# Kernel tuning notes

Measured on AMD Instinct MI355X. Metric: run time of the kernel, lower is better.

The kernel has to match this reference:

```python
import jax, jax.numpy as jnp
import numpy as np

N = 100000   # nodes
E = 1600000  # edges
D_IN = 4
D_H = 128
EPS = 1e-5

def setup_inputs() -> dict:
    key = jax.random.key(0)
    ks = jax.random.split(key, 4)
    x = jax.random.normal(ks[0], (N, D_IN), dtype=jnp.float32)
    edge_index = jax.random.randint(ks[1], (2, E), 0, N, dtype=jnp.int32)
    W0 = jax.random.normal(ks[2], (D_IN, D_H), dtype=jnp.float32) * 0.5
    b0 = jnp.zeros((D_H,), jnp.float32)
    W12 = jax.random.normal(ks[3], (2, D_H, D_H), dtype=jnp.float32) * (1.0 / np.sqrt(D_H))
    b12 = jnp.zeros((2, D_H), jnp.float32)
    gamma = jnp.ones((3, D_H), jnp.float32)   # GraphNorm weight
    beta = jnp.zeros((3, D_H), jnp.float32)   # GraphNorm bias
    alpha = jnp.ones((3, D_H), jnp.float32)   # GraphNorm mean_scale
    return dict(x=x, edge_index=edge_index, W0=W0, b0=b0, W12=W12, b12=b12,
                gamma=gamma, beta=beta, alpha=alpha)

def gcn_conv(x, src, dst, dinv, W, b):
    # PyG GCNConv: linear first, then D^-1/2 (A+I) D^-1/2 aggregation, bias after.
    h = x @ W                                  # [N, d_out]
    coef = dinv[src] * dinv[dst]               # [E]
    msg = h[src] * coef[:, None]               # [E, d_out] gather
    agg = jax.ops.segment_sum(msg, dst, num_segments=N)  # scatter-add
    agg = agg + h * (dinv * dinv)[:, None]     # self-loop contribution
    return agg + b

def graph_norm(x, g, be, a):
    # single-graph GraphNorm: gamma*(x - alpha*mu)/sqrt(E[(x-alpha*mu)^2]+eps)+beta
    mu = x.mean(axis=0)
    xc = x - a * mu
    var = (xc * xc).mean(axis=0)
    return g * xc * jax.lax.rsqrt(var + EPS) + be

def reference(x, edge_index, W0, b0, W12, b12, gamma, beta, alpha):
    src, dst = edge_index[0], edge_index[1]
    # degree with self loops (edge weight 1)
    deg = jax.ops.segment_sum(jnp.ones((E,), x.dtype), dst, num_segments=N) + 1.0
    dinv = jax.lax.rsqrt(deg)
    h = jax.nn.relu(graph_norm(gcn_conv(x, src, dst, dinv, W0, b0),
                               gamma[0], beta[0], alpha[0]))
    for i in range(2):  # fixed small layer loop
        h = jax.nn.relu(graph_norm(gcn_conv(h, src, dst, dinv, W12[i], b12[i]),
                                   gamma[i + 1], beta[i + 1], alpha[i + 1]))
    return h
```

## Files before the change

### kernel.cpp

```cpp
#include <hip/hip_runtime.h>


#define EPS_GN 1e-5f

typedef __attribute__((ext_vector_type(8))) short bf16x8;
typedef __attribute__((ext_vector_type(4))) float f32x4;

__device__ __forceinline__ float blo(unsigned u) { return __uint_as_float(u << 16); }
__device__ __forceinline__ float bhi(unsigned u) { return __uint_as_float(u & 0xffff0000u); }
__device__ __forceinline__ unsigned bf16rne(float f) {
  unsigned u = __float_as_uint(f);
  u += 0x7fff + ((u >> 16) & 1);
  return u >> 16;
}
__device__ __forceinline__ unsigned packbf(float x, float y) {
  return bf16rne(x) | (bf16rne(y) << 16);
}


__global__ __launch_bounds__(256) void k_count_p(const int* __restrict__ dst,
                                                 int* __restrict__ cnt, int E, int N) {
  int p = blockIdx.x & 7;
  int lo = (int)((long long)N * p >> 3), hi = (int)((long long)N * (p + 1) >> 3);
  int stride = (gridDim.x >> 3) * 256;
  for (int e = (blockIdx.x >> 3) * 256 + threadIdx.x; e < E; e += stride) {
    int d = dst[e];
    if (d >= lo && d < hi) atomicAdd(&cnt[d], 1);
  }
}

__global__ __launch_bounds__(256) void k_scan1(const int* __restrict__ cnt,
                                               int* __restrict__ rs,
                                               int* __restrict__ bsum, int N) {
  __shared__ int s[256];
  int t = threadIdx.x;
  int base = blockIdx.x * 1024 + t * 4;
  int c0 = (base + 0 < N) ? cnt[base + 0] : 0;
  int c1 = (base + 1 < N) ? cnt[base + 1] : 0;
  int c2 = (base + 2 < N) ? cnt[base + 2] : 0;
  int c3 = (base + 3 < N) ? cnt[base + 3] : 0;
  int tsum = c0 + c1 + c2 + c3;
  s[t] = tsum;
  __syncthreads();
  for (int off = 1; off < 256; off <<= 1) {
    int v = (t >= off) ? s[t - off] : 0;
    __syncthreads();
    s[t] += v;
    __syncthreads();
  }
  int excl = s[t] - tsum;
  if (t == 255) bsum[blockIdx.x] = s[255];
  int e0 = excl, e1 = e0 + c0, e2 = e1 + c1, e3 = e2 + c2;
  if (base + 0 < N) rs[base + 0] = e0;
  if (base + 1 < N) rs[base + 1] = e1;
  if (base + 2 < N) rs[base + 2] = e2;
  if (base + 3 < N) rs[base + 3] = e3;
}

__global__ __launch_bounds__(256) void k_scan2(const int* __restrict__ bsum,
                                               int* __restrict__ boff, int nblk) {
  __shared__ int s[256];
  int t = threadIdx.x;
  int v0 = (t < nblk) ? bsum[t] : 0;
  s[t] = v0;
  __syncthreads();
  for (int off = 1; off < 256; off <<= 1) {
    int v = (t >= off) ? s[t - off] : 0;
    __syncthreads();
    s[t] += v;
    __syncthreads();
  }
  if (t < nblk) boff[t] = s[t] - v0;
}

__global__ __launch_bounds__(256) void k_finalize(const int* __restrict__ cnt,
                                                  const int* __restrict__ boff,
                                                  int* __restrict__ rs,
                                                  int* __restrict__ cursor,
                                                  float* __restrict__ dinv, int N, int E) {
  int i = blockIdx.x * 256 + threadIdx.x;
  if (i == 0) rs[N] = E;
  if (i < N) {
    int v = rs[i] + boff[i >> 10];
    rs[i] = v;
    cursor[i] = v;
    dinv[i] = rsqrtf((float)cnt[i] + 1.0f);
  }
}

__global__ __launch_bounds__(256) void k_fill_p(const int* __restrict__ src,
                                                const int* __restrict__ dst,
                                                int* __restrict__ cursor,
                                                int* __restrict__ csr, int E, int N) {
  int p = blockIdx.x & 7;
  int lo = (int)((long long)N * p >> 3), hi = (int)((long long)N * (p + 1) >> 3);
  int stride = (gridDim.x >> 3) * 256;
  for (int e = (blockIdx.x >> 3) * 256 + threadIdx.x; e < E; e += stride) {
    int d = dst[e];
    if (d >= lo && d < hi) {
      int pos = atomicAdd(&cursor[d], 1);
      csr[pos] = src[e];
    }
  }
}


__global__ __launch_bounds__(256) void k_wt(const float* __restrict__ W12,
                                            unsigned short* __restrict__ WbT) {
  int o = blockIdx.x * 256 + threadIdx.x;
  int layer = o >> 14, r = o & 16383;
  int n = r >> 7, k = r & 127;
  WbT[o] = (unsigned short)bf16rne(W12[layer * 16384 + k * 128 + n]);
}


__global__ __launch_bounds__(256) void k_gemm0(const float* __restrict__ X,
                                               const float* __restrict__ W,
                                               const float* __restrict__ dinv,
                                               unsigned* __restrict__ H, int N) {
  __shared__ float Ws[4 * 128];
  int t = threadIdx.x;
  if (t < 128) {
    Ws[t] = W[t];
    Ws[128 + t] = W[128 + t];
    Ws[256 + t] = W[256 + t];
    Ws[384 + t] = W[384 + t];
  }
  __syncthreads();
  int r = t >> 6, l = t & 63;
  int row = blockIdx.x * 4 + r;
  if (row >= N) return;
  float4 xv = ((const float4*)X)[row];
  float di = dinv[row];
  int c0 = 2 * l, c1 = 2 * l + 1;
  float v0 = xv.x * Ws[c0] + xv.y * Ws[128 + c0] + xv.z * Ws[256 + c0] + xv.w * Ws[384 + c0];
  float v1 = xv.x * Ws[c1] + xv.y * Ws[128 + c1] + xv.z * Ws[256 + c1] + xv.w * Ws[384 + c1];
  H[(size_t)row * 64 + l] = packbf(di * v0, di * v1);
}

__global__ __launch_bounds__(256, 4) void k_gemm_mfma(const unsigned* __restrict__ AGGb,
                                                      const unsigned short* __restrict__ WbT,
                                                      const float* __restrict__ stats,
                                                      const float* __restrict__ bias,
                                                      const float* __restrict__ gamma,
                                                      const float* __restrict__ beta,
                                                      const float* __restrict__ alpha,
                                                      const float* __restrict__ dinv,
                                                      unsigned* __restrict__ H, int N,
                                                      float invN) {
  __shared__ float As[128], Bs[128];
  int t = threadIdx.x;
  if (t < 128) {
    float s1 = stats[t] * invN, s2 = stats[128 + t] * invN;
    float b = bias[t], a = alpha[t], g = gamma[t], be = beta[t];
    float mu = s1 + b;
    float E2 = s2 + 2.f * b * s1 + b * b;
    float var = E2 - (2.f * a - a * a) * mu * mu;
    float A = g * rsqrtf(var + EPS_GN);
    As[t] = A;
    Bs[t] = be - A * a * mu + A * b;
  }
  __syncthreads();
  int wv = t >> 6, l = t & 63;
  int r0 = blockIdx.x * 64 + wv * 16;
  if (r0 >= N) return;
  int m = l & 15, kb = l >> 4;

  f32x4 acc[8];
#pragma unroll
  for (int nt = 0; nt < 8; ++nt) acc[nt] = (f32x4){0.f, 0.f, 0.f, 0.f};

  const uint4* Arow = (const uint4*)(AGGb + (size_t)(r0 + m) * 64);

#pragma unroll
  for (int ks = 0; ks < 4; ++ks) {
    int k0 = ks * 32 + kb * 8;
    uint4 a_raw = Arow[ks * 4 + kb];
    float4 A0 = *reinterpret_cast<const float4*>(&As[k0]);
    float4 A1 = *reinterpret_cast<const float4*>(&As[k0 + 4]);
    float4 B0 = *reinterpret_cast<const float4*>(&Bs[k0]);
    float4 B1 = *reinterpret_cast<const float4*>(&Bs[k0 + 4]);
    bf16x8 bf[8];
#pragma unroll
    for (int nt = 0; nt < 8; ++nt)
      bf[nt] = *reinterpret_cast<const bf16x8*>(WbT + (size_t)(nt * 16 + m) * 128 + k0);
    float xr[8] = {blo(a_raw.x), bhi(a_raw.x), blo(a_raw.y), bhi(a_raw.y),
                   blo(a_raw.z), bhi(a_raw.z), blo(a_raw.w), bhi(a_raw.w)};
    float Aa[8] = {A0.x, A0.y, A0.z, A0.w, A1.x, A1.y, A1.z, A1.w};
    float Bb[8] = {B0.x, B0.y, B0.z, B0.w, B1.x, B1.y, B1.z, B1.w};
    bf16x8 af;
#pragma unroll
    for (int j = 0; j < 8; ++j) {
      float v = fmaf(Aa[j], xr[j], Bb[j]);
      v = v > 0.f ? v : 0.f;
      af[j] = (short)bf16rne(v);
    }
#pragma unroll
    for (int nt = 0; nt < 8; ++nt)
      acc[nt] = __builtin_amdgcn_mfma_f32_16x16x32_bf16(af, bf[nt], acc[nt], 0, 0, 0);
  }

  float dn[4];
#pragma unroll
  for (int r = 0; r < 4; ++r) dn[r] = dinv[r0 + kb * 4 + r];
  bool even = (l & 1) == 0;
#pragma unroll
  for (int nt = 0; nt < 8; ++nt) {
#pragma unroll
    for (int r = 0; r < 4; ++r) {
      float v = acc[nt][r] * dn[r];
      float pv = __shfl_xor(v, 1);
      if (even) {
        unsigned word = packbf(v, pv);
        H[(size_t)(r0 + kb * 4 + r) * 64 + nt * 8 + (m >> 1)] = word;
      }
    }
  }
}

__global__ __launch_bounds__(256) void k_gather(const uint4* __restrict__ H4,
                                                const int* __restrict__ rs,
                                                const int* __restrict__ csr,
                                                const float* __restrict__ dinv,
                                                unsigned* __restrict__ AGGb,
                                                float* __restrict__ stats, int N) {
  int wave = threadIdx.x >> 6, lane = threadIdx.x & 63;
  int g = lane >> 4, sl = lane & 15;
  float s1a = 0.f, s1b = 0.f, s2a = 0.f, s2b = 0.f;
  for (int n = blockIdx.x * 4 + wave; n < N; n += gridDim.x * 4) {
    int j0 = rs[n], j1 = rs[n + 1];
    int len = j1 - j0;
    int nb = (len + 4) >> 2;
    float acc[8];
#pragma unroll
    for (int i = 0; i < 8; ++i) acc[i] = 0.f;

    auto vsrc = [&](int b) -> int {
      int idx = b * 4 + g - 1;
      int jj = j0 + idx;
      jj = min(jj, j1 - 1);
      jj = max(jj, j0);
      int c = csr[jj];
      return (idx < 0) ? n : ((idx < len) ? c : N);
    };

    uint4 hA = H4[(size_t)vsrc(0) * 16 + sl];
    uint4 hB, hC, hD, hE;
    if (nb > 1) hB = H4[(size_t)vsrc(1) * 16 + sl];
    if (nb > 2) hC = H4[(size_t)vsrc(2) * 16 + sl];
    if (nb > 3) hD = H4[(size_t)vsrc(3) * 16 + sl];
    for (int b = 0; b < nb; ++b) {
      if (b + 4 < nb) hE = H4[(size_t)vsrc(b + 4) * 16 + sl];
      unsigned uu[4] = {hA.x, hA.y, hA.z, hA.w};
#pragma unroll
      for (int i = 0; i < 4; ++i) {
        acc[2 * i] += blo(uu[i]);
        acc[2 * i + 1] += bhi(uu[i]);
      }
      hA = hB;
      hB = hC;
      hC = hD;
      hD = hE;
    }
#pragma unroll
    for (int i = 0; i < 8; ++i) {
      acc[i] += __shfl_xor(acc[i], 16);
      acc[i] += __shfl_xor(acc[i], 32);
    }
    float dnv = dinv[n];
    float v0 = acc[2 * g] * dnv;
    float v1 = acc[2 * g + 1] * dnv;
    AGGb[(size_t)n * 64 + sl * 4 + g] = packbf(v0, v1);
    s1a += v0;
    s2a = fmaf(v0, v0, s2a);
    s1b += v1;
    s2b = fmaf(v1, v1, s2b);
  }
  __shared__ float sh[4][256];
  int col = sl * 8 + g * 2;
  sh[wave][col] = s1a;
  sh[wave][col + 1] = s1b;
  sh[wave][128 + col] = s2a;
  sh[wave][128 + col + 1] = s2b;
  __syncthreads();
  int t = threadIdx.x;
  float v = sh[0][t] + sh[1][t] + sh[2][t] + sh[3][t];
  atomicAdd(&stats[t], v);
}

__global__ __launch_bounds__(256) void k_norm(const unsigned* __restrict__ AGGb,
                                              const float* __restrict__ stats,
                                              const float* __restrict__ bias,
                                              const float* __restrict__ gamma,
                                              const float* __restrict__ beta,
                                              const float* __restrict__ alpha,
                                              float* __restrict__ OUT, int N, float invN) {
  int i = blockIdx.x * 256 + threadIdx.x;
  if (i >= N * 32) return;
  int c4 = i & 31;
  uint2 u = ((const uint2*)AGGb)[i];
  float vv[4] = {blo(u.x), bhi(u.x), blo(u.y), bhi(u.y)};
  float ov[4];
#pragma unroll
  for (int j = 0; j < 4; ++j) {
    int c = c4 * 4 + j;
    float s1 = stats[c] * invN, s2 = stats[128 + c] * invN;
    float b = bias[c], a = alpha[c], g = gamma[c], be = beta[c];
    float mu = s1 + b;
    float E2 = s2 + 2.f * b * s1 + b * b;
    float var = E2 - (2.f * a - a * a) * mu * mu;
    float A = g * rsqrtf(var + EPS_GN);
    float B = be - A * a * mu + A * b;
    float o = fmaf(A, vv[j], B);
    ov[j] = o > 0.f ? o : 0.f;
  }
  ((float4*)OUT)[i] = make_float4(ov[0], ov[1], ov[2], ov[3]);
}


extern "C" void kernel_launch(void* const* d_in, const int* in_sizes, int n_in,
                              void* d_out, int out_size, void* d_ws, size_t ws_size,
                              hipStream_t stream) {
  const float* x = (const float*)d_in[0];
  const int* ei = (const int*)d_in[1];
  const float* W0 = (const float*)d_in[2];
  const float* b0 = (const float*)d_in[3];
  const float* W12 = (const float*)d_in[4];
  const float* b12 = (const float*)d_in[5];
  const float* gamma = (const float*)d_in[6];
  const float* beta = (const float*)d_in[7];
  const float* alpha = (const float*)d_in[8];
  float* out = (float*)d_out;

  int N = in_sizes[0] / 4;
  int E = in_sizes[1] / 2;
  const int* srcArr = ei;
  const int* dstArr = ei + E;

  char* w = (char*)d_ws;
  auto alloc = [&](size_t bytes) {
    char* p = w;
    w += (bytes + 255) & ~(size_t)255;
    return p;
  };
  int* cnt = (int*)alloc((size_t)N * 4);
  float* stats = (float*)alloc(3 * 256 * 4);
  int* rs = (int*)alloc(((size_t)N + 1) * 4);
  int* cursor = (int*)alloc((size_t)N * 4);
  int* bsum = (int*)alloc(512);
  int* boff = (int*)alloc(512);
  unsigned short* WbT = (unsigned short*)alloc(2 * 16384 * 2);
  int* csr = (int*)alloc(((size_t)E + 8) * 4);
  float* dinv = (float*)alloc((size_t)N * 4);
  unsigned* Hb = (unsigned*)alloc(((size_t)N + 1) * 64 * 4);
  unsigned* AGGb = (unsigned*)alloc((size_t)N * 64 * 4);

  size_t zlen = (size_t)((char*)stats - (char*)cnt) + 3 * 256 * 4;
  hipMemsetAsync(cnt, 0, zlen, stream);
  hipMemsetAsync(Hb + (size_t)N * 64, 0, 256, stream);

  int nblk = (N + 1023) / 1024;
  k_wt<<<128, 256, 0, stream>>>(W12, WbT);
  k_count_p<<<2048, 256, 0, stream>>>(dstArr, cnt, E, N);
  k_scan1<<<nblk, 256, 0, stream>>>(cnt, rs, bsum, N);
  k_scan2<<<1, 256, 0, stream>>>(bsum, boff, nblk);
  k_finalize<<<(N + 255) / 256, 256, 0, stream>>>(cnt, boff, rs, cursor, dinv, N, E);
  k_fill_p<<<2048, 256, 0, stream>>>(srcArr, dstArr, cursor, csr, E, N);

  float invN = 1.0f / (float)N;
  int gGemm = (N + 63) / 64;
  const uint4* H4 = (const uint4*)Hb;

  k_gemm0<<<(N + 3) / 4, 256, 0, stream>>>(x, W0, dinv, Hb, N);
  k_gather<<<2048, 256, 0, stream>>>(H4, rs, csr, dinv, AGGb, stats, N);
  k_gemm_mfma<<<gGemm, 256, 0, stream>>>(AGGb, WbT, stats, b0, gamma, beta, alpha, dinv, Hb, N,
                                         invN);
  k_gather<<<2048, 256, 0, stream>>>(H4, rs, csr, dinv, AGGb, stats + 256, N);
  k_gemm_mfma<<<gGemm, 256, 0, stream>>>(AGGb, WbT + 16384, stats + 256, b12, gamma + 128,
                                         beta + 128, alpha + 128, dinv, Hb, N, invN);
  k_gather<<<2048, 256, 0, stream>>>(H4, rs, csr, dinv, AGGb, stats + 512, N);
  k_norm<<<(N * 32 + 255) / 256, 256, 0, stream>>>(AGGb, stats + 512, b12 + 128, gamma + 256,
                                                   beta + 256, alpha + 256, out, N, invN);
}
```

Before: 649.0 us.

## Store features in column-blocked layout so each gather pass touches one slice

Node features change from row-major [N,128] bf16 to eight column blocks of 16 channels, each stored as [ROWS,8] words. The gather kernel gives each block one column slice (blockIdx & 7), so one slice of about 3.2 MB is randomly gathered per pass and may stay in cache. Each wave now handles eight nodes, each with 8 lanes loading 32-bit words, instead of one node per wave loading 128-bit vectors. The GEMM, norm and gemm0 kernels are re-indexed to match, and the zero padding row moves into k_finalize. In exchange, every pass reads the CSR arrays eight times, and neighbor counts are padded to the wave's maximum degree.

```diff
diff --git a/kernel.cpp b/kernel.cpp
--- a/kernel.cpp
+++ b/kernel.cpp
@@ -77,9 +77,12 @@
                                                   const int* __restrict__ boff,
                                                   int* __restrict__ rs,
                                                   int* __restrict__ cursor,
-                                                  float* __restrict__ dinv, int N, int E) {
+                                                  float* __restrict__ dinv,
+                                                  unsigned* __restrict__ Hcb, int N, int E,
+                                                  int ROWS) {
   int i = blockIdx.x * 256 + threadIdx.x;
   if (i == 0) rs[N] = E;
+  if (i < 64) Hcb[((size_t)(i >> 3) * ROWS + N) * 8 + (i & 7)] = 0u;
   if (i < N) {
     int v = rs[i] + boff[i >> 10];
     rs[i] = v;
@@ -117,7 +120,7 @@
 __global__ __launch_bounds__(256) void k_gemm0(const float* __restrict__ X,
                                                const float* __restrict__ W,
                                                const float* __restrict__ dinv,
-                                               unsigned* __restrict__ H, int N) {
+                                               unsigned* __restrict__ Hcb, int N, int ROWS) {
   __shared__ float Ws[4 * 128];
   int t = threadIdx.x;
   if (t < 128) {
@@ -135,10 +138,10 @@
   int c0 = 2 * l, c1 = 2 * l + 1;
   float v0 = xv.x * Ws[c0] + xv.y * Ws[128 + c0] + xv.z * Ws[256 + c0] + xv.w * Ws[384 + c0];
   float v1 = xv.x * Ws[c1] + xv.y * Ws[128 + c1] + xv.z * Ws[256 + c1] + xv.w * Ws[384 + c1];
-  H[(size_t)row * 64 + l] = packbf(di * v0, di * v1);
-}
-
-__global__ __launch_bounds__(256, 4) void k_gemm_mfma(const unsigned* __restrict__ AGGb,
+  Hcb[((size_t)(l >> 3) * ROWS + row) * 8 + (l & 7)] = packbf(di * v0, di * v1);
+}
+
+__global__ __launch_bounds__(256, 4) void k_gemm_mfma(const unsigned* __restrict__ AGGcb,
                                                       const unsigned short* __restrict__ WbT,
                                                       const float* __restrict__ stats,
                                                       const float* __restrict__ bias,
@@ -146,8 +149,8 @@
                                                       const float* __restrict__ beta,
                                                       const float* __restrict__ alpha,
                                                       const float* __restrict__ dinv,
-                                                      unsigned* __restrict__ H, int N,
-                                                      float invN) {
+                                                      unsigned* __restrict__ Hcb, int N,
+                                                      int ROWS, float invN) {
   __shared__ float As[128], Bs[128];
   int t = threadIdx.x;
   if (t < 128) {
@@ -170,12 +173,12 @@
 #pragma unroll
   for (int nt = 0; nt < 8; ++nt) acc[nt] = (f32x4){0.f, 0.f, 0.f, 0.f};
 
-  const uint4* Arow = (const uint4*)(AGGb + (size_t)(r0 + m) * 64);
-
 #pragma unroll
   for (int ks = 0; ks < 4; ++ks) {
     int k0 = ks * 32 + kb * 8;
-    uint4 a_raw = Arow[ks * 4 + kb];
+    const uint4* pa = (const uint4*)(AGGcb + ((size_t)(2 * ks + (kb >> 1)) * ROWS + r0 + m) * 8 +
+                                     (kb & 1) * 4);
+    uint4 a_raw = pa[0];
     float4 A0 = *reinterpret_cast<const float4*>(&As[k0]);
     float4 A1 = *reinterpret_cast<const float4*>(&As[k0 + 4]);
     float4 B0 = *reinterpret_cast<const float4*>(&Bs[k0]);
@@ -212,93 +215,108 @@
       float pv = __shfl_xor(v, 1);
       if (even) {
         unsigned word = packbf(v, pv);
-        H[(size_t)(r0 + kb * 4 + r) * 64 + nt * 8 + (m >> 1)] = word;
+        Hcb[((size_t)nt * ROWS + r0 + kb * 4 + r) * 8 + (m >> 1)] = word;
       }
     }
   }
 }
 
-__global__ __launch_bounds__(256) void k_gather(const uint4* __restrict__ H4,
-                                                const int* __restrict__ rs,
-                                                const int* __restrict__ csr,
-                                                const float* __restrict__ dinv,
-                                                unsigned* __restrict__ AGGb,
-                                                float* __restrict__ stats, int N) {
-  int wave = threadIdx.x >> 6, lane = threadIdx.x & 63;
-  int g = lane >> 4, sl = lane & 15;
-  float s1a = 0.f, s1b = 0.f, s2a = 0.f, s2b = 0.f;
-  for (int n = blockIdx.x * 4 + wave; n < N; n += gridDim.x * 4) {
+__global__ __launch_bounds__(256) void k_gather_cb(const unsigned* __restrict__ Hcb,
+                                                   const int* __restrict__ rs,
+                                                   const int* __restrict__ csr,
+                                                   const float* __restrict__ dinv,
+                                                   unsigned* __restrict__ AGGcb,
+                                                   float* __restrict__ stats, int N, int ROWS) {
+  int t = threadIdx.x;
+  int wave = t >> 6, lane = t & 63;
+  int g = lane >> 3, cl = lane & 7;
+  int p = blockIdx.x & 7;
+  const unsigned* Hp = Hcb + (size_t)p * ROWS * 8;
+  unsigned* Ap = AGGcb + (size_t)p * ROWS * 8;
+  int q = blockIdx.x >> 3;
+  int nstride = (gridDim.x >> 3) * 32;
+  float s1a = 0.f, s2a = 0.f, s1b = 0.f, s2b = 0.f;
+  for (int n0 = (q * 4 + wave) * 8; n0 < N; n0 += nstride) {
+    int n = n0 + g;
     int j0 = rs[n], j1 = rs[n + 1];
     int len = j1 - j0;
-    int nb = (len + 4) >> 2;
-    float acc[8];
-#pragma unroll
-    for (int i = 0; i < 8; ++i) acc[i] = 0.f;
-
-    auto vsrc = [&](int b) -> int {
-      int idx = b * 4 + g - 1;
-      int jj = j0 + idx;
+    int ml = len;
+    ml = max(ml, __shfl_xor(ml, 8));
+    ml = max(ml, __shfl_xor(ml, 16));
+    ml = max(ml, __shfl_xor(ml, 32));
+    int cnt = ml + 1;
+    float a0 = 0.f, a1 = 0.f;
+    auto vsrc = [&](int j) -> int {
+      int jj = j0 + j;
       jj = min(jj, j1 - 1);
       jj = max(jj, j0);
       int c = csr[jj];
-      return (idx < 0) ? n : ((idx < len) ? c : N);
+      return (j < 0) ? n : ((j < len) ? c : N);
     };
-
-    uint4 hA = H4[(size_t)vsrc(0) * 16 + sl];
-    uint4 hB, hC, hD, hE;
-    if (nb > 1) hB = H4[(size_t)vsrc(1) * 16 + sl];
-    if (nb > 2) hC = H4[(size_t)vsrc(2) * 16 + sl];
-    if (nb > 3) hD = H4[(size_t)vsrc(3) * 16 + sl];
-    for (int b = 0; b < nb; ++b) {
-      if (b + 4 < nb) hE = H4[(size_t)vsrc(b + 4) * 16 + sl];
-      unsigned uu[4] = {hA.x, hA.y, hA.z, hA.w};
-#pragma unroll
-      for (int i = 0; i < 4; ++i) {
-        acc[2 * i] += blo(uu[i]);
-        acc[2 * i + 1] += bhi(uu[i]);
-      }
-      hA = hB;
-      hB = hC;
-      hC = hD;
-      hD = hE;
+    unsigned rA = Hp[(size_t)vsrc(-1) * 8 + cl];
+    unsigned rB, rC, rD, rE;
+    if (cnt > 1) rB = Hp[(size_t)vsrc(0) * 8 + cl];
+    if (cnt > 2) rC = Hp[(size_t)vsrc(1) * 8 + cl];
+    if (cnt > 3) rD = Hp[(size_t)vsrc(2) * 8 + cl];
+    for (int it = 0; it < cnt; ++it) {
+      if (it + 4 < cnt) rE = Hp[(size_t)vsrc(it + 3) * 8 + cl];
+      a0 += blo(rA);
+      a1 += bhi(rA);
+      rA = rB;
+      rB = rC;
+      rC = rD;
+      rD = rE;
     }
-#pragma unroll
-    for (int i = 0; i < 8; ++i) {
-      acc[i] += __shfl_xor(acc[i], 16);
-      acc[i] += __shfl_xor(acc[i], 32);
-    }
-    float dnv = dinv[n];
-    float v0 = acc[2 * g] * dnv;
-    float v1 = acc[2 * g + 1] * dnv;
-    AGGb[(size_t)n * 64 + sl * 4 + g] = packbf(v0, v1);
+    float dn = dinv[n];
+    float v0 = a0 * dn, v1 = a1 * dn;
+    Ap[(size_t)n * 8 + cl] = packbf(v0, v1);
     s1a += v0;
     s2a = fmaf(v0, v0, s2a);
     s1b += v1;
     s2b = fmaf(v1, v1, s2b);
   }
-  __shared__ float sh[4][256];
-  int col = sl * 8 + g * 2;
-  sh[wave][col] = s1a;
-  sh[wave][col + 1] = s1b;
-  sh[wave][128 + col] = s2a;
-  sh[wave][128 + col + 1] = s2b;
+  s1a += __shfl_xor(s1a, 8);
+  s1a += __shfl_xor(s1a, 16);
+  s1a += __shfl_xor(s1a, 32);
+  s2a += __shfl_xor(s2a, 8);
+  s2a += __shfl_xor(s2a, 16);
+  s2a += __shfl_xor(s2a, 32);
+  s1b += __shfl_xor(s1b, 8);
+  s1b += __shfl_xor(s1b, 16);
+  s1b += __shfl_xor(s1b, 32);
+  s2b += __shfl_xor(s2b, 8);
+  s2b += __shfl_xor(s2b, 16);
+  s2b += __shfl_xor(s2b, 32);
+  __shared__ float sh[4][32];
+  if (g == 0) {
+    sh[wave][2 * cl] = s1a;
+    sh[wave][2 * cl + 1] = s1b;
+    sh[wave][16 + 2 * cl] = s2a;
+    sh[wave][16 + 2 * cl + 1] = s2b;
+  }
   __syncthreads();
-  int t = threadIdx.x;
-  float v = sh[0][t] + sh[1][t] + sh[2][t] + sh[3][t];
-  atomicAdd(&stats[t], v);
-}
-
-__global__ __launch_bounds__(256) void k_norm(const unsigned* __restrict__ AGGb,
+  if (t < 32) {
+    float v = sh[0][t] + sh[1][t] + sh[2][t] + sh[3][t];
+    if (t < 16)
+      atomicAdd(&stats[p * 16 + t], v);
+    else
+      atomicAdd(&stats[128 + p * 16 + (t - 16)], v);
+  }
+}
+
+__global__ __launch_bounds__(256) void k_norm(const unsigned* __restrict__ AGGcb,
                                               const float* __restrict__ stats,
                                               const float* __restrict__ bias,
                                               const float* __restrict__ gamma,
                                               const float* __restrict__ beta,
                                               const float* __restrict__ alpha,
-                                              float* __restrict__ OUT, int N, float invN) {
+                                              float* __restrict__ OUT, int N, int ROWS,
+                                              float invN) {
   int i = blockIdx.x * 256 + threadIdx.x;
   if (i >= N * 32) return;
-  int c4 = i & 31;
-  uint2 u = ((const uint2*)AGGb)[i];
+  int row = i >> 5, c4 = i & 31;
+  int blk = c4 >> 2, off = (2 * c4) & 7;
+  uint2 u = *(const uint2*)(AGGcb + ((size_t)blk * ROWS + row) * 8 + off);
   float vv[4] = {blo(u.x), bhi(u.x), blo(u.y), bhi(u.y)};
   float ov[4];
 #pragma unroll
@@ -334,6 +352,7 @@
 
   int N = in_sizes[0] / 4;
   int E = in_sizes[1] / 2;
+  int ROWS = N + 1;
   const int* srcArr = ei;
   const int* dstArr = ei + E;
 
@@ -352,33 +371,31 @@
   unsigned short* WbT = (unsigned short*)alloc(2 * 16384 * 2);
   int* csr = (int*)alloc(((size_t)E + 8) * 4);
   float* dinv = (float*)alloc((size_t)N * 4);
-  unsigned* Hb = (unsigned*)alloc(((size_t)N + 1) * 64 * 4);
-  unsigned* AGGb = (unsigned*)alloc((size_t)N * 64 * 4);
+  unsigned* Hcb = (unsigned*)alloc((size_t)ROWS * 64 * 4);
+  unsigned* AGGcb = (unsigned*)alloc((size_t)ROWS * 64 * 4);
 
   size_t zlen = (size_t)((char*)stats - (char*)cnt) + 3 * 256 * 4;
   hipMemsetAsync(cnt, 0, zlen, stream);
-  hipMemsetAsync(Hb + (size_t)N * 64, 0, 256, stream);
 
   int nblk = (N + 1023) / 1024;
   k_wt<<<128, 256, 0, stream>>>(W12, WbT);
   k_count_p<<<2048, 256, 0, stream>>>(dstArr, cnt, E, N);
   k_scan1<<<nblk, 256, 0, stream>>>(cnt, rs, bsum, N);
   k_scan2<<<1, 256, 0, stream>>>(bsum, boff, nblk);
-  k_finalize<<<(N + 255) / 256, 256, 0, stream>>>(cnt, boff, rs, cursor, dinv, N, E);
+  k_finalize<<<(N + 255) / 256, 256, 0, stream>>>(cnt, boff, rs, cursor, dinv, Hcb, N, E, ROWS);
   k_fill_p<<<2048, 256, 0, stream>>>(srcArr, dstArr, cursor, csr, E, N);
 
   float invN = 1.0f / (float)N;
   int gGemm = (N + 63) / 64;
-  const uint4* H4 = (const uint4*)Hb;
-
-  k_gemm0<<<(N + 3) / 4, 256, 0, stream>>>(x, W0, dinv, Hb, N);
-  k_gather<<<2048, 256, 0, stream>>>(H4, rs, csr, dinv, AGGb, stats, N);
-  k_gemm_mfma<<<gGemm, 256, 0, stream>>>(AGGb, WbT, stats, b0, gamma, beta, alpha, dinv, Hb, N,
-                                         invN);
-  k_gather<<<2048, 256, 0, stream>>>(H4, rs, csr, dinv, AGGb, stats + 256, N);
-  k_gemm_mfma<<<gGemm, 256, 0, stream>>>(AGGb, WbT + 16384, stats + 256, b12, gamma + 128,
-                                         beta + 128, alpha + 128, dinv, Hb, N, invN);
-  k_gather<<<2048, 256, 0, stream>>>(H4, rs, csr, dinv, AGGb, stats + 512, N);
-  k_norm<<<(N * 32 + 255) / 256, 256, 0, stream>>>(AGGb, stats + 512, b12 + 128, gamma + 256,
-                                                   beta + 256, alpha + 256, out, N, invN);
-}
+
+  k_gemm0<<<(N + 3) / 4, 256, 0, stream>>>(x, W0, dinv, Hcb, N, ROWS);
+  k_gather_cb<<<2048, 256, 0, stream>>>(Hcb, rs, csr, dinv, AGGcb, stats, N, ROWS);
+  k_gemm_mfma<<<gGemm, 256, 0, stream>>>(AGGcb, WbT, stats, b0, gamma, beta, alpha, dinv, Hcb, N,
+                                         ROWS, invN);
+  k_gather_cb<<<2048, 256, 0, stream>>>(Hcb, rs, csr, dinv, AGGcb, stats + 256, N, ROWS);
+  k_gemm_mfma<<<gGemm, 256, 0, stream>>>(AGGcb, WbT + 16384, stats + 256, b12, gamma + 128,
+                                         beta + 128, alpha + 128, dinv, Hcb, N, ROWS, invN);
+  k_gather_cb<<<2048, 256, 0, stream>>>(Hcb, rs, csr, dinv, AGGcb, stats + 512, N, ROWS);
+  k_norm<<<(N * 32 + 255) / 256, 256, 0, stream>>>(AGGcb, stats + 512, b12 + 128, gamma + 256,
+                                                   beta + 256, alpha + 256, out, N, ROWS, invN);
+}
```

Result: slower. 835.9 us (+28.8%).
